# Kernel optimization log

Measured on AMD Instinct MI355X. Metric: run time of the kernel, lower is better.

## Reference

```python
import jax, jax.numpy as jnp
import numpy as np

N, E, F_IN, F_HID, K = 100000, 1600000, 64, 64, 6


def setup_inputs() -> dict:
    key = jax.random.key(0)
    k1, k2, k3, k4, k5 = jax.random.split(key, 5)
    x = jax.random.normal(k1, (N, F_IN), dtype=jnp.float32)
    # edges with no self-loops (PyG ChebConv removes self loops before normalization)
    src = jax.random.randint(k2, (E,), 0, N, dtype=jnp.int32)
    off = jax.random.randint(k3, (E,), 1, N, dtype=jnp.int32)
    dst = (src + off) % N
    edge_index = jnp.stack([src, dst], axis=0)
    # Glorot-ish init for the K Chebyshev weight matrices
    W = jax.random.normal(k4, (K, F_IN, F_HID), dtype=jnp.float32) * (1.0 / np.sqrt(F_IN))
    b = jax.random.normal(k5, (F_HID,), dtype=jnp.float32) * 0.01
    return {"x": x, "edge_index": edge_index, "W": W, "b": b}


def reference(x, edge_index, W, b):
    # ChebConv with sym normalization, lambda_max = 2.0 (PyG default):
    # scaled Laplacian L_hat = 2*L/lambda_max - I = -D^{-1/2} A D^{-1/2} (zero diagonal)
    row = edge_index[0].astype(jnp.int32)  # source j
    col = edge_index[1].astype(jnp.int32)  # target i
    n = x.shape[0]
    deg = jax.ops.segment_sum(jnp.ones_like(row, dtype=x.dtype), row, num_segments=n)
    dinv = jnp.where(deg > 0, jax.lax.rsqrt(deg), jnp.zeros_like(deg))
    w = -(dinv[row] * dinv[col])  # [E] edge weights of L_hat

    def prop(h):  # h: [N, F] -> L_hat @ h via gather-scale-scatter
        return jax.ops.segment_sum(w[:, None] * h[row], col, num_segments=n)

    # Chebyshev recurrence: Tx_0 = x, Tx_1 = L_hat x, Tx_k = 2 L_hat Tx_{k-1} - Tx_{k-2}
    Tx0 = x
    out = Tx0 @ W[0]
    Tx1 = prop(Tx0)
    out = out + Tx1 @ W[1]
    for k in range(2, W.shape[0]):
        Tx2 = 2.0 * prop(Tx1) - Tx0
        out = out + Tx2 @ W[k]
        Tx0, Tx1 = Tx1, Tx2
    return jax.nn.relu(out + b)
```

## Files before the change

kernel.cpp:

```cpp
#include <hip/hip_runtime.h>


constexpr int F = 64;
constexpr int SCAN_ELEMS = 1024;
constexpr int BSH = 9;
constexpr int EPB = 2048;
constexpr int PNPW = 8;

typedef __attribute__((ext_vector_type(8))) short short8;
typedef __attribute__((ext_vector_type(4))) float floatx4;
typedef __attribute__((ext_vector_type(2))) float floatx2;

#if defined(__has_builtin)
#if __has_builtin(__builtin_amdgcn_cvt_pk_f32_fp8) && __has_builtin(__builtin_amdgcn_cvt_pk_fp8_f32)
#define HAVE_FP8 1
#endif
#endif
#ifndef HAVE_FP8
#define HAVE_FP8 0
#endif

__device__ __forceinline__ unsigned short f_to_bf(float f) {
    unsigned u = __float_as_uint(f);
    u += 0x7FFFu + ((u >> 16) & 1u);
    return (unsigned short)(u >> 16);
}
__device__ __forceinline__ float bf_to_f(unsigned short s) {
    return __uint_as_float(((unsigned)s) << 16);
}
__device__ __forceinline__ float4 bf4_to_f4(ushort4 u) {
    float4 f;
    f.x = bf_to_f(u.x); f.y = bf_to_f(u.y); f.z = bf_to_f(u.z); f.w = bf_to_f(u.w);
    return f;
}

#if HAVE_FP8
__device__ __forceinline__ float4 fp8x4_to_f4(unsigned u) {
    floatx2 lo = __builtin_amdgcn_cvt_pk_f32_fp8((int)u, false);
    floatx2 hi = __builtin_amdgcn_cvt_pk_f32_fp8((int)u, true);
    float4 f;
    f.x = lo.x; f.y = lo.y; f.z = hi.x; f.w = hi.y;
    return f;
}
__device__ __forceinline__ unsigned f4_to_fp8x4(float a, float b, float c, float d) {
    int pk = 0;
    pk = __builtin_amdgcn_cvt_pk_fp8_f32(a, b, pk, false);
    pk = __builtin_amdgcn_cvt_pk_fp8_f32(c, d, pk, true);
    return (unsigned)pk;
}
#else
__device__ __forceinline__ float4 fp8x4_to_f4(unsigned u) { return make_float4(0, 0, 0, 0); }
__device__ __forceinline__ unsigned f4_to_fp8x4(float a, float b, float c, float d) { return 0; }
#endif

__global__ void hist2_kernel(const int* __restrict__ row, const int* __restrict__ col,
                             int* __restrict__ gcH, int* __restrict__ gcS,
                             int P, int G, int E) {
    __shared__ int hH[256], hS[256];
    const int tid = threadIdx.x, blk = blockIdx.x;
    hH[tid] = 0; hS[tid] = 0;
    __syncthreads();
    const int start = blk * EPB + tid * 8;
    if (start + 7 < E) {
        const int4 c0 = *(const int4*)(col + start);
        const int4 c1 = *(const int4*)(col + start + 4);
        const int4 r0 = *(const int4*)(row + start);
        const int4 r1 = *(const int4*)(row + start + 4);
        atomicAdd(&hH[c0.x >> BSH], 1); atomicAdd(&hH[c0.y >> BSH], 1);
        atomicAdd(&hH[c0.z >> BSH], 1); atomicAdd(&hH[c0.w >> BSH], 1);
        atomicAdd(&hH[c1.x >> BSH], 1); atomicAdd(&hH[c1.y >> BSH], 1);
        atomicAdd(&hH[c1.z >> BSH], 1); atomicAdd(&hH[c1.w >> BSH], 1);
        atomicAdd(&hS[r0.x >> BSH], 1); atomicAdd(&hS[r0.y >> BSH], 1);
        atomicAdd(&hS[r0.z >> BSH], 1); atomicAdd(&hS[r0.w >> BSH], 1);
        atomicAdd(&hS[r1.x >> BSH], 1); atomicAdd(&hS[r1.y >> BSH], 1);
        atomicAdd(&hS[r1.z >> BSH], 1); atomicAdd(&hS[r1.w >> BSH], 1);
    } else {
        for (int k = start; k < E && k < start + 8; ++k) {
            atomicAdd(&hH[col[k] >> BSH], 1);
            atomicAdd(&hS[row[k] >> BSH], 1);
        }
    }
    __syncthreads();
    if (tid < P) {
        gcH[(size_t)tid * G + blk] = hH[tid];
        gcS[(size_t)tid * G + blk] = hS[tid];
    }
}

__device__ __forceinline__ int4 load_cnt4(const int* __restrict__ cnt, int i, int N) {
    int4 v = make_int4(0, 0, 0, 0);
    if (i + 3 < N) {
        v = *(const int4*)(cnt + i);
    } else {
        if (i + 0 < N) v.x = cnt[i + 0];
        if (i + 1 < N) v.y = cnt[i + 1];
        if (i + 2 < N) v.z = cnt[i + 2];
        if (i + 3 < N) v.w = cnt[i + 3];
    }
    return v;
}

__global__ void scan1_kernel(const int* __restrict__ cnt, int* __restrict__ bsum, int N) {
    const int tid = threadIdx.x;
    const int i = blockIdx.x * SCAN_ELEMS + tid * 4;
    int4 v = load_cnt4(cnt, i, N);
    int s = v.x + v.y + v.z + v.w;
#pragma unroll
    for (int off = 1; off < 64; off <<= 1) s += __shfl_xor(s, off);
    __shared__ int ws[4];
    if ((tid & 63) == 0) ws[tid >> 6] = s;
    __syncthreads();
    if (tid == 0) bsum[blockIdx.x] = ws[0] + ws[1] + ws[2] + ws[3];
}

__global__ void scan2_kernel(const int* __restrict__ bsum, int* __restrict__ boff,
                             int* __restrict__ total_out, int nb) {
    const int tid = threadIdx.x;
    const int lane = tid & 63, w = tid >> 6;
    int v = (tid < nb) ? bsum[tid] : 0;
    int inc = v;
#pragma unroll
    for (int off = 1; off < 64; off <<= 1) {
        int t = __shfl_up(inc, off);
        if (lane >= off) inc += t;
    }
    __shared__ int wsum[4];
    if (lane == 63) wsum[w] = inc;
    __syncthreads();
    int wo = 0;
    for (int k = 0; k < w; ++k) wo += wsum[k];
    const int excl = wo + inc - v;
    if (tid < nb) boff[tid] = excl;
    if (tid == nb - 1) *total_out = excl + v;
}

__global__ void scan3_kernel(const int* __restrict__ cnt, const int* __restrict__ boff,
                             int* __restrict__ dst, int N) {
    const int tid = threadIdx.x;
    const int lane = tid & 63, w = tid >> 6;
    const int i = blockIdx.x * SCAN_ELEMS + tid * 4;
    int4 v = load_cnt4(cnt, i, N);
    const int s = v.x + v.y + v.z + v.w;
    int inc = s;
#pragma unroll
    for (int off = 1; off < 64; off <<= 1) {
        int t = __shfl_up(inc, off);
        if (lane >= off) inc += t;
    }
    __shared__ int wsum[4];
    if (lane == 63) wsum[w] = inc;
    __syncthreads();
    int wo = 0;
    for (int k = 0; k < w; ++k) wo += wsum[k];
    const int r0 = boff[blockIdx.x] + wo + inc - s;
    const int r1 = r0 + v.x, r2 = r1 + v.y, r3 = r2 + v.z;
    if (i + 3 < N) {
        *(int4*)(dst + i) = make_int4(r0, r1, r2, r3);
    } else {
        if (i + 0 < N) dst[i + 0] = r0;
        if (i + 1 < N) dst[i + 1] = r1;
        if (i + 2 < N) dst[i + 2] = r2;
        if (i + 3 < N) dst[i + 3] = r3;
    }
}

__global__ void part2_kernel(const int* __restrict__ row, const int* __restrict__ col,
                             const int* __restrict__ goH, const int* __restrict__ goS,
                             int2* __restrict__ partH, int* __restrict__ partS,
                             int P, int G, int E) {
    __shared__ int cH[256], cS[256];
    const int tid = threadIdx.x, blk = blockIdx.x;
    if (tid < P) {
        cH[tid] = goH[(size_t)tid * G + blk];
        cS[tid] = goS[(size_t)tid * G + blk];
    }
    __syncthreads();
    const int start = blk * EPB + tid * 8;
    for (int k = start; k < E && k < start + 8; ++k) {
        const int c = col[k], r = row[k];
        const int posH = atomicAdd(&cH[c >> BSH], 1);
        partH[posH] = make_int2(c, r);
        const int posS = atomicAdd(&cS[r >> BSH], 1);
        partS[posS] = r;
    }
}

__global__ void bucketC_kernel(const int2* __restrict__ part, const int* __restrict__ goff,
                               int* __restrict__ rowptr, int* __restrict__ csr,
                               int P, int G, int N, int E) {
    __shared__ int cnt[512];
    __shared__ int excl[512];
    __shared__ int wsum[4];
    const int tid = threadIdx.x;
    const int b = blockIdx.x;
    const int base_node = b << BSH;
    const int nn = min(512, N - base_node);
    const int estart = goff[(size_t)b * G];
    const int eend = (b + 1 < P) ? goff[(size_t)(b + 1) * G] : E;

    cnt[tid] = 0; cnt[tid + 256] = 0;
    __syncthreads();
    for (int i = estart + tid; i < eend; i += 256)
        atomicAdd(&cnt[part[i].x - base_node], 1);
    __syncthreads();
    {
        const int lane = tid & 63, w = tid >> 6;
        const int a0 = cnt[2 * tid], a1 = cnt[2 * tid + 1];
        const int ps = a0 + a1;
        int inc = ps;
#pragma unroll
        for (int off = 1; off < 64; off <<= 1) {
            int t = __shfl_up(inc, off);
            if (lane >= off) inc += t;
        }
        if (lane == 63) wsum[w] = inc;
        __syncthreads();
        int wo = 0;
        for (int k = 0; k < w; ++k) wo += wsum[k];
        const int ep = wo + inc - ps;
        excl[2 * tid] = ep;
        excl[2 * tid + 1] = ep + a0;
    }
    __syncthreads();
    if (tid < nn) rowptr[base_node + tid] = estart + excl[tid];
    for (int ln = 256 + tid; ln < nn; ln += 256) rowptr[base_node + ln] = estart + excl[ln];
    if (b == P - 1 && tid == 0) rowptr[N] = E;
    cnt[tid] = 0; cnt[tid + 256] = 0;
    __syncthreads();
    for (int i = estart + tid; i < eend; i += 256) {
        const int2 e = part[i];
        const int ln = e.x - base_node;
        const int pos = atomicAdd(&cnt[ln], 1);
        csr[estart + excl[ln] + pos] = e.y;
    }
}

__global__ void bucketD_kernel(const int* __restrict__ partS, const int* __restrict__ goffS,
                               float* __restrict__ dinv, float* __restrict__ dinv2,
                               float* __restrict__ rdinv, int P, int G, int N, int E) {
    __shared__ int cnt[512];
    const int tid = threadIdx.x;
    const int b = blockIdx.x;
    const int base_node = b << BSH;
    const int nn = min(512, N - base_node);
    const int estart = goffS[(size_t)b * G];
    const int eend = (b + 1 < P) ? goffS[(size_t)(b + 1) * G] : E;
    cnt[tid] = 0; cnt[tid + 256] = 0;
    __syncthreads();
    for (int i = estart + tid; i < eend; i += 256)
        atomicAdd(&cnt[partS[i] - base_node], 1);
    __syncthreads();
    for (int l = tid; l < nn; l += 256) {
        const int dI = cnt[l];
        const float d = (float)dI;
        const bool ok = dI > 0;
        dinv[base_node + l]  = ok ? rsqrtf(d) : 0.0f;
        dinv2[base_node + l] = ok ? 1.0f / d : 0.0f;
        rdinv[base_node + l] = ok ? sqrtf(d) : 0.0f;
    }
}

__global__ void init_s0_kernel(const float* __restrict__ dinv, const float* __restrict__ x,
                               unsigned short* __restrict__ S0b, unsigned char* __restrict__ S0f8,
                               int NF, int write8) {
    int i = blockIdx.x * blockDim.x + threadIdx.x;
    int j = i * 4;
    if (j >= NF) return;
    const float dv = dinv[j >> 6];
    const float4 v = *(const float4*)(x + j);
    const float a = dv * v.x, bb = dv * v.y, c = dv * v.z, d = dv * v.w;
    ushort4 u;
    u.x = f_to_bf(a); u.y = f_to_bf(bb); u.z = f_to_bf(c); u.w = f_to_bf(d);
    *(ushort4*)(S0b + j) = u;
    if (write8) *(unsigned*)(S0f8 + j) = f4_to_fp8x4(a, bb, c, d);
}

template <int FIRST>
__global__ __launch_bounds__(256, 8)
void prop_g4(const int* __restrict__ rowptr, const int* __restrict__ csr,
             const float* __restrict__ dinv2, const unsigned short* __restrict__ Sprev,
             const unsigned short* __restrict__ Sm2, unsigned short* __restrict__ Sk, int N) {
    const int lane = threadIdx.x & 63;
    const int g16 = lane & 48;
    const int fl = lane & 15;
    const int wave = threadIdx.x >> 6;
    const int wbase = (blockIdx.x * 4 + wave) * PNPW;
    for (int j = 0; j < PNPW; j += 4) {
        const int n = wbase + j + (g16 >> 4);
        const bool nv = n < N;
        const int nc = nv ? n : N - 1;
        const int s = rowptr[nc], e = rowptr[nc + 1];
        const int len = e - s;
        float4 acc = {0.f, 0.f, 0.f, 0.f};
        for (int c = 0; c < len; c += 16) {
            const int ii = s + c + fl;
            const int idxv = csr[ii < e ? ii : e - 1];
            const int mm = min(16, len - c);
            for (int jj = 0; jj < mm; jj += 4) {
                const int i0 = __shfl(idxv, g16 + jj + 0);
                const int i1 = __shfl(idxv, g16 + jj + 1);
                const int i2 = __shfl(idxv, g16 + jj + 2);
                const int i3 = __shfl(idxv, g16 + jj + 3);
                const ushort4 u0 = *(const ushort4*)(Sprev + (size_t)i0 * F + fl * 4);
                const ushort4 u1 = *(const ushort4*)(Sprev + (size_t)i1 * F + fl * 4);
                const ushort4 u2 = *(const ushort4*)(Sprev + (size_t)i2 * F + fl * 4);
                const ushort4 u3 = *(const ushort4*)(Sprev + (size_t)i3 * F + fl * 4);
                {
                    const float4 v = bf4_to_f4(u0);
                    acc.x += v.x; acc.y += v.y; acc.z += v.z; acc.w += v.w;
                }
                if (jj + 1 < mm) {
                    const float4 v = bf4_to_f4(u1);
                    acc.x += v.x; acc.y += v.y; acc.z += v.z; acc.w += v.w;
                }
                if (jj + 2 < mm) {
                    const float4 v = bf4_to_f4(u2);
                    acc.x += v.x; acc.y += v.y; acc.z += v.z; acc.w += v.w;
                }
                if (jj + 3 < mm) {
                    const float4 v = bf4_to_f4(u3);
                    acc.x += v.x; acc.y += v.y; acc.z += v.z; acc.w += v.w;
                }
            }
        }
        if (nv) {
            const float d2 = dinv2[n];
            float4 sn;
            if (FIRST) {
                sn.x = -d2 * acc.x; sn.y = -d2 * acc.y;
                sn.z = -d2 * acc.z; sn.w = -d2 * acc.w;
            } else {
                const float4 m2 = bf4_to_f4(*(const ushort4*)(Sm2 + (size_t)n * F + fl * 4));
                sn.x = -2.f * d2 * acc.x - m2.x; sn.y = -2.f * d2 * acc.y - m2.y;
                sn.z = -2.f * d2 * acc.z - m2.z; sn.w = -2.f * d2 * acc.w - m2.w;
            }
            ushort4 o;
            o.x = f_to_bf(sn.x); o.y = f_to_bf(sn.y);
            o.z = f_to_bf(sn.z); o.w = f_to_bf(sn.w);
            *(ushort4*)(Sk + (size_t)n * F + fl * 4) = o;
        }
    }
}

template <int FIRST, int W8>
__global__ __launch_bounds__(256, 8)
void prop_f8(const int* __restrict__ rowptr, const int* __restrict__ csr,
             const float* __restrict__ dinv2, const unsigned char* __restrict__ S8prev,
             const unsigned short* __restrict__ Sm2, unsigned short* __restrict__ Sk,
             unsigned char* __restrict__ Sk8, int N) {
    const int lane = threadIdx.x & 63;
    const int g16 = lane & 48;
    const int fl = lane & 15;
    const int wave = threadIdx.x >> 6;
    const int wbase = (blockIdx.x * 4 + wave) * PNPW;
    for (int j = 0; j < PNPW; j += 4) {
        const int n = wbase + j + (g16 >> 4);
        const bool nv = n < N;
        const int nc = nv ? n : N - 1;
        const int s = rowptr[nc], e = rowptr[nc + 1];
        const int len = e - s;
        float4 acc = {0.f, 0.f, 0.f, 0.f};
        for (int c = 0; c < len; c += 16) {
            const int ii = s + c + fl;
            const int idxv = csr[ii < e ? ii : e - 1];
            const int mm = min(16, len - c);
            for (int jj = 0; jj < mm; jj += 4) {
                const int i0 = __shfl(idxv, g16 + jj + 0);
                const int i1 = __shfl(idxv, g16 + jj + 1);
                const int i2 = __shfl(idxv, g16 + jj + 2);
                const int i3 = __shfl(idxv, g16 + jj + 3);
                const unsigned u0 = *(const unsigned*)(S8prev + (size_t)i0 * F + fl * 4);
                const unsigned u1 = *(const unsigned*)(S8prev + (size_t)i1 * F + fl * 4);
                const unsigned u2 = *(const unsigned*)(S8prev + (size_t)i2 * F + fl * 4);
                const unsigned u3 = *(const unsigned*)(S8prev + (size_t)i3 * F + fl * 4);
                {
                    const float4 v = fp8x4_to_f4(u0);
                    acc.x += v.x; acc.y += v.y; acc.z += v.z; acc.w += v.w;
                }
                if (jj + 1 < mm) {
                    const float4 v = fp8x4_to_f4(u1);
                    acc.x += v.x; acc.y += v.y; acc.z += v.z; acc.w += v.w;
                }
                if (jj + 2 < mm) {
                    const float4 v = fp8x4_to_f4(u2);
                    acc.x += v.x; acc.y += v.y; acc.z += v.z; acc.w += v.w;
                }
                if (jj + 3 < mm) {
                    const float4 v = fp8x4_to_f4(u3);
                    acc.x += v.x; acc.y += v.y; acc.z += v.z; acc.w += v.w;
                }
            }
        }
        if (nv) {
            const float d2 = dinv2[n];
            float4 sn;
            if (FIRST) {
                sn.x = -d2 * acc.x; sn.y = -d2 * acc.y;
                sn.z = -d2 * acc.z; sn.w = -d2 * acc.w;
            } else {
                const float4 m2 = bf4_to_f4(*(const ushort4*)(Sm2 + (size_t)n * F + fl * 4));
                sn.x = -2.f * d2 * acc.x - m2.x; sn.y = -2.f * d2 * acc.y - m2.y;
                sn.z = -2.f * d2 * acc.z - m2.z; sn.w = -2.f * d2 * acc.w - m2.w;
            }
            ushort4 o;
            o.x = f_to_bf(sn.x); o.y = f_to_bf(sn.y);
            o.z = f_to_bf(sn.z); o.w = f_to_bf(sn.w);
            *(ushort4*)(Sk + (size_t)n * F + fl * 4) = o;
            if (W8) *(unsigned*)(Sk8 + (size_t)n * F + fl * 4) = f4_to_fp8x4(sn.x, sn.y, sn.z, sn.w);
        }
    }
}

__global__ void wfrag_kernel(const float* __restrict__ W, unsigned short* __restrict__ Wfrag) {
    const int idx = blockIdx.x * blockDim.x + threadIdx.x;
    if (idx >= 4 * 12 * 64) return;
    const int lane = idx & 63;
    const int s = (idx >> 6) % 12;
    const int ft = idx / (64 * 12);
    const int n = ft * 16 + (lane & 15);
    const int quad = lane >> 4;
    unsigned short v[8];
#pragma unroll
    for (int j = 0; j < 8; ++j) {
        const int kg = s * 32 + quad * 8 + j;
        const int kk = kg >> 6, f = kg & 63;
        v[j] = f_to_bf(W[kk * F * F + f * F + n]);
    }
    ushort4 lo = {v[0], v[1], v[2], v[3]};
    ushort4 hi = {v[4], v[5], v[6], v[7]};
    *(ushort4*)(Wfrag + (size_t)idx * 8) = lo;
    *(ushort4*)(Wfrag + (size_t)idx * 8 + 4) = hi;
}

__global__ __launch_bounds__(256, 3)
void mfma_out_kernel(const float* __restrict__ x, const unsigned short* __restrict__ Sstack,
                     const unsigned short* __restrict__ Wfrag, const float* __restrict__ rdinv,
                     const float* __restrict__ dinv2, const float* __restrict__ W,
                     const float* __restrict__ b, float* __restrict__ out, int N, int NF) {
    const int lane = threadIdx.x & 63;
    const int wave = threadIdx.x >> 6;
    const int quad = lane >> 4;
    const int fl = lane & 15;
    const int tm = (blockIdx.x * 4 + wave) * 16;
    if (tm >= N) return;
    const int ma = tm + fl;
    const int mac = ma < N ? ma : N - 1;

    const unsigned short* sa = Sstack + (size_t)mac * F + quad * 8;

    short8 Afr[12];
#pragma unroll
    for (int s = 0; s < 12; ++s) {
        const int kk = s >> 1, f0 = (s & 1) * 32;
        Afr[s] = *(const short8*)(sa + (size_t)kk * NF + f0);
    }

    floatx4 C0 = {0.f, 0.f, 0.f, 0.f};
    floatx4 C1 = {0.f, 0.f, 0.f, 0.f};
    floatx4 C2 = {0.f, 0.f, 0.f, 0.f};
    floatx4 C3 = {0.f, 0.f, 0.f, 0.f};
    const unsigned short* wf = Wfrag + (size_t)lane * 8;
#pragma unroll
    for (int s = 0; s < 12; ++s) {
        const short8 B0 = *(const short8*)(wf + (size_t)(0 * 12 + s) * 64 * 8);
        const short8 B1 = *(const short8*)(wf + (size_t)(1 * 12 + s) * 64 * 8);
        const short8 B2 = *(const short8*)(wf + (size_t)(2 * 12 + s) * 64 * 8);
        const short8 B3 = *(const short8*)(wf + (size_t)(3 * 12 + s) * 64 * 8);
        C0 = __builtin_amdgcn_mfma_f32_16x16x32_bf16(Afr[s], B0, C0, 0, 0, 0);
        C1 = __builtin_amdgcn_mfma_f32_16x16x32_bf16(Afr[s], B1, C1, 0, 0, 0);
        C2 = __builtin_amdgcn_mfma_f32_16x16x32_bf16(Afr[s], B2, C2, 0, 0, 0);
        C3 = __builtin_amdgcn_mfma_f32_16x16x32_bf16(Afr[s], B3, C3, 0, 0, 0);
    }

    const float bl0 = b[0 * 16 + fl];
    const float bl1 = b[1 * 16 + fl];
    const float bl2 = b[2 * 16 + fl];
    const float bl3 = b[3 * 16 + fl];

#pragma unroll
    for (int r = 0; r < 4; ++r) {
        const int m = tm + quad * 4 + r;
        if (m >= N) continue;
        const float rs = rdinv[m];
        const bool z = (dinv2[m] == 0.0f);
        float v0 = rs * C0[r], v1 = rs * C1[r], v2 = rs * C2[r], v3 = rs * C3[r];
        if (z) {
            const float* xr = x + (size_t)m * F;
            float f0 = 0.f, f1 = 0.f, f2 = 0.f, f3 = 0.f;
            for (int f = 0; f < F; ++f) {
                const float xv = xr[f];
                const float* w0 = W + 0 * F * F + f * F;
                const float* w2 = W + 2 * F * F + f * F;
                const float* w4 = W + 4 * F * F + f * F;
                f0 += xv * (w0[0 * 16 + fl] - w2[0 * 16 + fl] + w4[0 * 16 + fl]);
                f1 += xv * (w0[1 * 16 + fl] - w2[1 * 16 + fl] + w4[1 * 16 + fl]);
                f2 += xv * (w0[2 * 16 + fl] - w2[2 * 16 + fl] + w4[2 * 16 + fl]);
                f3 += xv * (w0[3 * 16 + fl] - w2[3 * 16 + fl] + w4[3 * 16 + fl]);
            }
            v0 = f0; v1 = f1; v2 = f2; v3 = f3;
        }
        float* orow = out + (size_t)m * F;
        orow[0 * 16 + fl] = fmaxf(v0 + bl0, 0.f);
        orow[1 * 16 + fl] = fmaxf(v1 + bl1, 0.f);
        orow[2 * 16 + fl] = fmaxf(v2 + bl2, 0.f);
        orow[3 * 16 + fl] = fmaxf(v3 + bl3, 0.f);
    }
}

extern "C" void kernel_launch(void* const* d_in, const int* in_sizes, int n_in,
                              void* d_out, int out_size, void* d_ws, size_t ws_size,
                              hipStream_t stream) {
    const float* x = (const float*)d_in[0];
    const int* ei = (const int*)d_in[1];
    const float* W = (const float*)d_in[2];
    const float* b = (const float*)d_in[3];

    const int N = in_sizes[0] / F;
    const int E = in_sizes[1] / 2;
    const int NF = N * F;
    const int* row = ei;
    const int* col = ei + E;

    const int P = (N + 511) >> BSH;
    const int G = (E + EPB - 1) / EPB;
    const int M = P * G;

    char* p = (char*)d_ws;
    auto alloc = [&](size_t bytes) {
        char* r = p;
        p += (bytes + 63) & ~(size_t)63;
        return r;
    };
    float* dinv   = (float*)alloc((size_t)N * sizeof(float));
    float* dinv2  = (float*)alloc((size_t)N * sizeof(float));
    float* rdinv  = (float*)alloc((size_t)N * sizeof(float));
    int*   rowptr = (int*)alloc((size_t)(N + 1) * sizeof(int));
    int*   bsum   = (int*)alloc(256 * sizeof(int));
    int*   boff   = (int*)alloc(256 * sizeof(int));
    int*   totS   = (int*)alloc(64);
    int*   gcH    = (int*)alloc((size_t)M * sizeof(int));
    int*   goH    = (int*)alloc((size_t)M * sizeof(int));
    int*   gcS    = (int*)alloc((size_t)M * sizeof(int));
    int*   goS    = (int*)alloc((size_t)M * sizeof(int));
    int*   csr    = (int*)alloc((size_t)E * sizeof(int));
    unsigned short* Sstack = (unsigned short*)alloc((size_t)6 * NF * sizeof(unsigned short));
    unsigned short* Wfrag  = (unsigned short*)alloc((size_t)4 * 12 * 64 * 8 * sizeof(unsigned short));
    unsigned char* F8A = (unsigned char*)alloc((size_t)NF);
    unsigned char* F8B = (unsigned char*)alloc((size_t)NF);
    const size_t needed = (size_t)(p - (char*)d_ws);
    const bool pathA = HAVE_FP8 && ws_size >= needed;
    int2* partH = (int2*)Sstack;
    int*  partS = (int*)(Sstack + (size_t)NF);
    float* out = (float*)d_out;

    const int B = 256;
    const int nsbM = (M + SCAN_ELEMS - 1) / SCAN_ELEMS;
    const int pgrid = (N + 4 * PNPW - 1) / (4 * PNPW);

    hist2_kernel<<<G, B, 0, stream>>>(row, col, gcH, gcS, P, G, E);
    scan1_kernel<<<nsbM, B, 0, stream>>>(gcH, bsum, M);
    scan2_kernel<<<1, B, 0, stream>>>(bsum, boff, rowptr + N, nsbM);
    scan3_kernel<<<nsbM, B, 0, stream>>>(gcH, boff, goH, M);
    scan1_kernel<<<nsbM, B, 0, stream>>>(gcS, bsum, M);
    scan2_kernel<<<1, B, 0, stream>>>(bsum, boff, totS, nsbM);
    scan3_kernel<<<nsbM, B, 0, stream>>>(gcS, boff, goS, M);
    part2_kernel<<<G, B, 0, stream>>>(row, col, goH, goS, partH, partS, P, G, E);
    bucketC_kernel<<<P, B, 0, stream>>>(partH, goH, rowptr, csr, P, G, N, E);
    bucketD_kernel<<<P, B, 0, stream>>>(partS, goS, dinv, dinv2, rdinv, P, G, N, E);

    wfrag_kernel<<<(4 * 12 * 64 + B - 1) / B, B, 0, stream>>>(W, Wfrag);
    init_s0_kernel<<<(NF / 4 + B - 1) / B, B, 0, stream>>>(dinv, x, Sstack, F8A, NF,
                                                           pathA ? 1 : 0);
    unsigned short* S1 = Sstack + (size_t)1 * NF;
    unsigned short* S2 = Sstack + (size_t)2 * NF;
    unsigned short* S3 = Sstack + (size_t)3 * NF;
    unsigned short* S4 = Sstack + (size_t)4 * NF;
    unsigned short* S5 = Sstack + (size_t)5 * NF;
    if (pathA) {
        prop_f8<1, 1><<<pgrid, B, 0, stream>>>(rowptr, csr, dinv2, F8A, Sstack, S1, F8B, N);
        prop_f8<0, 1><<<pgrid, B, 0, stream>>>(rowptr, csr, dinv2, F8B, Sstack, S2, F8A, N);
        prop_f8<0, 1><<<pgrid, B, 0, stream>>>(rowptr, csr, dinv2, F8A, S1, S3, F8B, N);
        prop_f8<0, 1><<<pgrid, B, 0, stream>>>(rowptr, csr, dinv2, F8B, S2, S4, F8A, N);
        prop_f8<0, 0><<<pgrid, B, 0, stream>>>(rowptr, csr, dinv2, F8A, S3, S5, F8B, N);
    } else {
        prop_g4<1><<<pgrid, B, 0, stream>>>(rowptr, csr, dinv2, Sstack, Sstack, S1, N);
        prop_g4<0><<<pgrid, B, 0, stream>>>(rowptr, csr, dinv2, S1, Sstack, S2, N);
        prop_g4<0><<<pgrid, B, 0, stream>>>(rowptr, csr, dinv2, S2, S1, S3, N);
        prop_g4<0><<<pgrid, B, 0, stream>>>(rowptr, csr, dinv2, S3, S2, S4, N);
        prop_g4<0><<<pgrid, B, 0, stream>>>(rowptr, csr, dinv2, S4, S3, S5, N);
    }
    mfma_out_kernel<<<(N + 63) / 64, 256, 0, stream>>>(x, Sstack, Wfrag, rdinv, dinv2,
                                                       W, b, out, N, NF);
}
```

Before: 369.5 us.

## Pack bucket edges into one int and issue 16 gathers per chunk

```diff
diff --git a/kernel.cpp b/kernel.cpp
--- a/kernel.cpp
+++ b/kernel.cpp
@@ -166,7 +166,7 @@
 
 __global__ void part2_kernel(const int* __restrict__ row, const int* __restrict__ col,
                              const int* __restrict__ goH, const int* __restrict__ goS,
-                             int2* __restrict__ partH, int* __restrict__ partS,
+                             int* __restrict__ partH, int* __restrict__ partS,
                              int P, int G, int E) {
     __shared__ int cH[256], cS[256];
     const int tid = threadIdx.x, blk = blockIdx.x;
@@ -179,13 +179,13 @@
     for (int k = start; k < E && k < start + 8; ++k) {
         const int c = col[k], r = row[k];
         const int posH = atomicAdd(&cH[c >> BSH], 1);
-        partH[posH] = make_int2(c, r);
+        partH[posH] = ((c & ((1 << BSH) - 1)) << 23) | r;
         const int posS = atomicAdd(&cS[r >> BSH], 1);
         partS[posS] = r;
     }
 }
 
-__global__ void bucketC_kernel(const int2* __restrict__ part, const int* __restrict__ goff,
+__global__ void bucketC_kernel(const int* __restrict__ part, const int* __restrict__ goff,
                                int* __restrict__ rowptr, int* __restrict__ csr,
                                int P, int G, int N, int E) {
     __shared__ int cnt[512];
@@ -201,7 +201,7 @@
     cnt[tid] = 0; cnt[tid + 256] = 0;
     __syncthreads();
     for (int i = estart + tid; i < eend; i += 256)
-        atomicAdd(&cnt[part[i].x - base_node], 1);
+        atomicAdd(&cnt[((unsigned)part[i]) >> 23], 1);
     __syncthreads();
     {
         const int lane = tid & 63, w = tid >> 6;
@@ -228,10 +228,10 @@
     cnt[tid] = 0; cnt[tid + 256] = 0;
     __syncthreads();
     for (int i = estart + tid; i < eend; i += 256) {
-        const int2 e = part[i];
-        const int ln = e.x - base_node;
+        const int pk = part[i];
+        const int ln = ((unsigned)pk) >> 23;
         const int pos = atomicAdd(&cnt[ln], 1);
-        csr[estart + excl[ln] + pos] = e.y;
+        csr[estart + excl[ln] + pos] = pk & 0x7FFFFF;
     }
 }
 
@@ -276,7 +276,7 @@
 }
 
 template <int FIRST>
-__global__ __launch_bounds__(256, 8)
+__global__ __launch_bounds__(256, 6)
 void prop_g4(const int* __restrict__ rowptr, const int* __restrict__ csr,
              const float* __restrict__ dinv2, const unsigned short* __restrict__ Sprev,
              const unsigned short* __restrict__ Sm2, unsigned short* __restrict__ Sk, int N) {
@@ -296,29 +296,16 @@
             const int ii = s + c + fl;
             const int idxv = csr[ii < e ? ii : e - 1];
             const int mm = min(16, len - c);
-            for (int jj = 0; jj < mm; jj += 4) {
-                const int i0 = __shfl(idxv, g16 + jj + 0);
-                const int i1 = __shfl(idxv, g16 + jj + 1);
-                const int i2 = __shfl(idxv, g16 + jj + 2);
-                const int i3 = __shfl(idxv, g16 + jj + 3);
-                const ushort4 u0 = *(const ushort4*)(Sprev + (size_t)i0 * F + fl * 4);
-                const ushort4 u1 = *(const ushort4*)(Sprev + (size_t)i1 * F + fl * 4);
-                const ushort4 u2 = *(const ushort4*)(Sprev + (size_t)i2 * F + fl * 4);
-                const ushort4 u3 = *(const ushort4*)(Sprev + (size_t)i3 * F + fl * 4);
-                {
-                    const float4 v = bf4_to_f4(u0);
-                    acc.x += v.x; acc.y += v.y; acc.z += v.z; acc.w += v.w;
-                }
-                if (jj + 1 < mm) {
-                    const float4 v = bf4_to_f4(u1);
-                    acc.x += v.x; acc.y += v.y; acc.z += v.z; acc.w += v.w;
-                }
-                if (jj + 2 < mm) {
-                    const float4 v = bf4_to_f4(u2);
-                    acc.x += v.x; acc.y += v.y; acc.z += v.z; acc.w += v.w;
-                }
-                if (jj + 3 < mm) {
-                    const float4 v = bf4_to_f4(u3);
+            ushort4 u[16];
+#pragma unroll
+            for (int t = 0; t < 16; ++t) {
+                const int it = __shfl(idxv, g16 + t);
+                u[t] = *(const ushort4*)(Sprev + (size_t)it * F + fl * 4);
+            }
+#pragma unroll
+            for (int t = 0; t < 16; ++t) {
+                if (t < mm) {
+                    const float4 v = bf4_to_f4(u[t]);
                     acc.x += v.x; acc.y += v.y; acc.z += v.z; acc.w += v.w;
                 }
             }
@@ -343,7 +330,7 @@
 }
 
 template <int FIRST, int W8>
-__global__ __launch_bounds__(256, 8)
+__global__ __launch_bounds__(256, 6)
 void prop_f8(const int* __restrict__ rowptr, const int* __restrict__ csr,
              const float* __restrict__ dinv2, const unsigned char* __restrict__ S8prev,
              const unsigned short* __restrict__ Sm2, unsigned short* __restrict__ Sk,
@@ -364,29 +351,16 @@
             const int ii = s + c + fl;
             const int idxv = csr[ii < e ? ii : e - 1];
             const int mm = min(16, len - c);
-            for (int jj = 0; jj < mm; jj += 4) {
-                const int i0 = __shfl(idxv, g16 + jj + 0);
-                const int i1 = __shfl(idxv, g16 + jj + 1);
-                const int i2 = __shfl(idxv, g16 + jj + 2);
-                const int i3 = __shfl(idxv, g16 + jj + 3);
-                const unsigned u0 = *(const unsigned*)(S8prev + (size_t)i0 * F + fl * 4);
-                const unsigned u1 = *(const unsigned*)(S8prev + (size_t)i1 * F + fl * 4);
-                const unsigned u2 = *(const unsigned*)(S8prev + (size_t)i2 * F + fl * 4);
-                const unsigned u3 = *(const unsigned*)(S8prev + (size_t)i3 * F + fl * 4);
-                {
-                    const float4 v = fp8x4_to_f4(u0);
-                    acc.x += v.x; acc.y += v.y; acc.z += v.z; acc.w += v.w;
-                }
-                if (jj + 1 < mm) {
-                    const float4 v = fp8x4_to_f4(u1);
-                    acc.x += v.x; acc.y += v.y; acc.z += v.z; acc.w += v.w;
-                }
-                if (jj + 2 < mm) {
-                    const float4 v = fp8x4_to_f4(u2);
-                    acc.x += v.x; acc.y += v.y; acc.z += v.z; acc.w += v.w;
-                }
-                if (jj + 3 < mm) {
-                    const float4 v = fp8x4_to_f4(u3);
+            unsigned u[16];
+#pragma unroll
+            for (int t = 0; t < 16; ++t) {
+                const int it = __shfl(idxv, g16 + t);
+                u[t] = *(const unsigned*)(S8prev + (size_t)it * F + fl * 4);
+            }
+#pragma unroll
+            for (int t = 0; t < 16; ++t) {
+                if (t < mm) {
+                    const float4 v = fp8x4_to_f4(u[t]);
                     acc.x += v.x; acc.y += v.y; acc.z += v.z; acc.w += v.w;
                 }
             }
@@ -549,8 +523,8 @@
     unsigned char* F8B = (unsigned char*)alloc((size_t)NF);
     const size_t needed = (size_t)(p - (char*)d_ws);
     const bool pathA = HAVE_FP8 && ws_size >= needed;
-    int2* partH = (int2*)Sstack;
-    int*  partS = (int*)(Sstack + (size_t)NF);
+    int* partH = (int*)Sstack;
+    int* partS = (int*)(Sstack + (size_t)NF);
     float* out = (float*)d_out;
 
     const int B = 256;
```

After: 368.0 us. Within noise of the previous version (-0.4%).
